# Optimization experiments

Hardware: AMD Instinct MI355X
Metric: run time of the kernel (lower is better)

Reference implementation:

```python
import jax, jax.numpy as jnp
import numpy as np

NF = 64  # n_features
NL = 3   # n_layers


def setup_inputs() -> dict:
    key = jax.random.key(0)
    ks = jax.random.split(key, 16)
    B, G, P = 4, 512, 512
    obs = jax.random.randint(ks[0], (B, G, P), 0, 3).astype(jnp.float32)

    def w(k, shape, fan_in):
        return (jax.random.normal(k, shape, jnp.float32) / np.sqrt(fan_in)).astype(jnp.float32)

    return {
        "obs": obs,
        "W_init_g": w(ks[1], (1, NF), 1),          # node_init_embedding_layer_g Linear(1,64)
        "W_init_p": w(ks[2], (1, NF), 1),
        "W_ee_g": w(ks[3], (1, NF - 1), 1),        # edge_embedding_NN (n_obs_in_p -> 63)
        "W_ef_g": w(ks[4], (NF, NF), NF),          # edge_feature_NN (64 -> 64)
        "W_ee_p": w(ks[5], (1, NF - 1), 1),
        "W_ef_p": w(ks[6], (NF, NF), NF),
        "W_msg_g": w(ks[7], (NL, 2 * NF, NF), 2 * NF),
        "W_upd_g": w(ks[8], (NL, 2 * NF, NF), 2 * NF),
        "W_msg_p": w(ks[9], (NL, 2 * NF, NF), 2 * NF),
        "W_upd_p": w(ks[10], (NL, 2 * NF, NF), 2 * NF),
        "W_pool_g": w(ks[11], (NF, NF), NF),
        "W_pool_p": w(ks[12], (NF, NF), NF),
        "W_ro": w(ks[13], (2 * NF, 1), 2 * NF),    # readout Linear(128,1,bias=True)
        "b_ro": jnp.zeros((1,), jnp.float32),
    }


def _norms(a):
    # torch get_normalisation is under no_grad
    n = jax.lax.stop_gradient(jnp.sum(a != 0, axis=-1, keepdims=True).astype(a.dtype))
    return n, jnp.where(n == 0, 1.0, n)


def _edge_emb(node_feat_opp, adj, norm, nf1, W_ee, W_ef):
    # node_feat_opp: [B,C,1], adj: [B,R,C] -> edge tensor [B,R,C,1]
    mask = (adj != 0).astype(adj.dtype)
    ef = node_feat_opp[:, None, :, :] * mask[..., None]          # [B,R,C,1]
    ee = jax.nn.relu(jnp.einsum('brci,ie->brce', ef, W_ee))      # [B,R,C,63]
    emb = ee.sum(axis=2) / nf1                                   # [B,R,63]
    x = jnp.concatenate([emb, norm / jnp.max(nf1)], axis=-1)     # [B,R,64]
    return jax.nn.relu(x @ W_ef)


def reference(obs, W_init_g, W_init_p, W_ee_g, W_ef_g, W_ee_p, W_ef_p,
              W_msg_g, W_upd_g, W_msg_p, W_upd_p, W_pool_g, W_pool_p, W_ro, b_ro):
    relu = jax.nn.relu
    adj = obs                                  # n_obs_in_g == 1 -> no leading node features
    adjT = jnp.swapaxes(adj, -1, -2)
    B, G, P = adj.shape
    norm_g, nf1_g = _norms(adj)
    norm_p, nf1_p = _norms(adjT)
    nf_g = norm_g / P                          # node_features_g [B,G,1]
    nf_p = norm_p / G                          # node_features_p [B,P,1]
    h_g = relu(nf_g @ W_init_g)                # [B,G,64]
    h_p = relu(nf_p @ W_init_p)                # [B,P,64]
    e_g = _edge_emb(nf_p, adj, norm_g, nf1_g, W_ee_g, W_ef_g)
    e_p = _edge_emb(nf_g, adjT, norm_p, nf1_p, W_ee_p, W_ef_p)
    for i in range(NL):
        agg_g = (adj @ h_p) / nf1_g
        agg_p = (adjT @ h_g) / nf1_p
        m_g = relu(jnp.concatenate([agg_g, e_g], axis=-1) @ W_msg_g[i])
        m_p = relu(jnp.concatenate([agg_p, e_p], axis=-1) @ W_msg_p[i])
        h_g_new = relu(jnp.concatenate([h_g, m_g], axis=-1) @ W_upd_g[i])
        h_p_new = relu(jnp.concatenate([h_p, m_p], axis=-1) @ W_upd_p[i])
        h_g, h_p = h_g_new, h_p_new
    hp_g = (h_g.sum(axis=1) / G) @ W_pool_g    # [B,64]
    hp_p = (h_p.sum(axis=1) / P) @ W_pool_p
    hp = relu(hp_g + hp_p)
    f_pooled = jnp.broadcast_to(hp[:, None, :], h_g.shape)
    feats = relu(jnp.concatenate([f_pooled, h_g], axis=-1))      # [B,G,128]
    out = feats @ W_ro + b_ro                  # [B,G,1]
    return out[..., 0]                         # torch .squeeze() -> [B,G]
```

## Files before the change

### kernel.cpp

```cpp
#include <hip/hip_runtime.h>

#define NF 64

#define OFF_U       8194
#define OFF_NPG     9216
#define OFF_NPP     25600
#define OFF_HA_G    41984
#define OFF_HA_P    173056
#define OFF_HB_G    304128
#define OFF_HB_P    435200
#define OFF_EG      566272
#define OFF_EP      697344
#define OFF_AFRAG   2162688
#define OFF_HFA     3211264
#define OFF_HFB     3735552
#define OFF_WF      4259840
#define OFF_HPART   4358144

typedef __attribute__((ext_vector_type(8))) short bf16x8;
typedef __attribute__((ext_vector_type(4))) float f32x4;

static __device__ __forceinline__ float wave_sum(float v) {
    for (int off = 32; off; off >>= 1) v += __shfl_down(v, off, 64);
    return v;
}
static __device__ __forceinline__ float wave_max(float v) {
    for (int off = 32; off; off >>= 1) v = fmaxf(v, __shfl_down(v, off, 64));
    return v;
}
static __device__ __forceinline__ unsigned short f2bf(float x) {
    unsigned u = __float_as_uint(x);
    return (unsigned short)((u + 0x7FFFu + ((u >> 16) & 1u)) >> 16);
}

__global__ __launch_bounds__(256) void k_prep(const float* __restrict__ obs,
        float* __restrict__ ws,
        const float* __restrict__ Wm_g, const float* __restrict__ Wu_g,
        const float* __restrict__ Wm_p, const float* __restrict__ Wu_p,
        const float* __restrict__ Wee_g, const float* __restrict__ Wef_g,
        const float* __restrict__ Wee_p, const float* __restrict__ Wef_p) {
    __shared__ float tile[64][65];
    __shared__ float cc[4][64];
    int b = blockIdx.y, t = threadIdx.x;
    int tg = blockIdx.x >> 3, tp = blockIdx.x & 7;
    int g0 = tg * 64, p0 = tp * 64;
    int c = t & 63, q = t >> 6;
    const float* src = obs + ((size_t)b * 512 + g0) * 512 + p0;
    float colcnt = 0.f;
#pragma unroll
    for (int i = 0; i < 16; ++i) {
        int r = q + 4 * i;
        float v = src[(size_t)r * 512 + c];
        tile[r][c] = v;
        bool nz = (v != 0.f);
        colcnt += nz ? 1.f : 0.f;
        unsigned long long mask = __ballot(nz);
        if (c == 0)
            ws[OFF_NPG + tp * 2048 + b * 512 + g0 + r] = (float)__popcll(mask);
    }
    cc[q][c] = colcnt;
    __syncthreads();
    if (q == 0)
        ws[OFF_NPP + tg * 2048 + b * 512 + p0 + c] =
            cc[0][c] + cc[1][c] + cc[2][c] + cc[3][c];
    int ri = c & 15, kq = c >> 4;
    unsigned short* afg = (unsigned short*)(ws + OFF_AFRAG);
    unsigned short* afp = afg + 1048576;
    int rt_g = b * 32 + tg * 4 + q;
    int rt_p = b * 32 + tp * 4 + q;
#pragma unroll
    for (int ks2 = 0; ks2 < 2; ++ks2) {
        int ks_g = tp * 2 + ks2;
        int ks_p = tg * 2 + ks2;
        bf16x8 og, op;
#pragma unroll
        for (int i = 0; i < 8; ++i) {
            og[i] = (short)f2bf(tile[q * 16 + ri][ks2 * 32 + kq * 8 + i]);
            op[i] = (short)f2bf(tile[ks2 * 32 + kq * 8 + i][q * 16 + ri]);
        }
        *(bf16x8*)(afg + ((size_t)(rt_g * 16 + ks_g) * 64 + c) * 8) = og;
        *(bf16x8*)(afp + ((size_t)(rt_p * 16 + ks_p) * 64 + c) * 8) = op;
    }
    int lin = b * 64 + blockIdx.x;
    if (lin < 48) {
        int mat = lin >> 2, ks2 = lin & 3;
        int side = mat / 6, m = (mat / 3) & 1, layer = mat % 3;
        const float* W = (side ? (m ? Wu_p : Wm_p) : (m ? Wu_g : Wm_g)) + layer * 8192;
        int ftq = t >> 6, lane = t & 63;
        int f = ftq * 16 + (lane & 15);
        int kbase = ks2 * 32 + ((lane >> 4) & 3) * 8;
        bf16x8 oh, ol;
#pragma unroll
        for (int i = 0; i < 8; ++i) {
            float v = W[(kbase + i) * 64 + f];
            unsigned short hi = f2bf(v);
            oh[i] = (short)hi;
            ol[i] = (short)f2bf(v - __uint_as_float((unsigned)hi << 16));
        }
        unsigned short* WF = (unsigned short*)(ws + OFF_WF);
        *(bf16x8*)(WF + (((size_t)(mat * 2 + 0) * 4 + ks2) * 4 + ftq) * 512 + lane * 8) = oh;
        *(bf16x8*)(WF + (((size_t)(mat * 2 + 1) * 4 + ks2) * 4 + ftq) * 512 + lane * 8) = ol;
    } else if (lin == 48 && t < 128) {
        int side = t >> 6, f = t & 63;
        const float* Wee = side ? Wee_p : Wee_g;
        const float* Wef = side ? Wef_p : Wef_g;
        float u = 0.f;
#pragma unroll
        for (int e = 0; e < 63; ++e) u += fmaxf(Wee[e], 0.f) * Wef[e * 64 + f];
        ws[OFF_U + t] = u;
    }
}

__global__ __launch_bounds__(256) void k_init_l0(float* __restrict__ ws,
        const float* __restrict__ Wi_g, const float* __restrict__ Wi_p,
        const float* __restrict__ Wef_g, const float* __restrict__ Wef_p) {
    __shared__ float normall[2048];
    __shared__ float nopp[512];
    __shared__ float redm[4];
    __shared__ float sred[4][16], wred[4][16];
    __shared__ float s_l[16], w_l[16];
    __shared__ float xe[16][68], xh[16][68], xa[16][68], xm[16][68];
    int bid = blockIdx.x, side = bid >> 7, rt = bid & 127;
    int lr0 = rt * 16, b = rt >> 5;
    int t = threadIdx.x, lane = t & 63, w = t >> 6;
    const float* pown = ws + (side ? OFF_NPP : OFF_NPG);
    const float* popp = ws + (side ? OFF_NPG : OFF_NPP) + b * 512;
#pragma unroll
    for (int i = 0; i < 8; ++i) {
        int r = t + 256 * i;
        float s = 0.f;
#pragma unroll
        for (int j = 0; j < 8; ++j) s += pown[j * 2048 + r];
        normall[r] = s;
    }
#pragma unroll
    for (int i = 0; i < 2; ++i) {
        int r = t + 256 * i;
        float s = 0.f;
#pragma unroll
        for (int j = 0; j < 8; ++j) s += popp[j * 2048 + r];
        nopp[r] = s;
    }
    __syncthreads();
    float m = 0.f;
#pragma unroll
    for (int i = 0; i < 8; ++i) m = fmaxf(m, normall[t + 256 * i]);
    m = wave_max(m);
    if (lane == 0) redm[w] = m;
    const unsigned short* af = (const unsigned short*)(ws + OFF_AFRAG)
                               + (size_t)side * 1048576;
    int kq = lane >> 4;
    float sacc = 0.f, wacc = 0.f;
#pragma unroll
    for (int kk = 0; kk < 4; ++kk) {
        int ks = w * 4 + kk;
        bf16x8 a = *(const bf16x8*)(af + ((size_t)(rt * 16 + ks) * 64 + lane) * 8);
#pragma unroll
        for (int i = 0; i < 8; ++i)
            if (a[i] != 0) {
                float nv = nopp[ks * 32 + kq * 8 + i];
                sacc += nv;
                float av = __uint_as_float((unsigned)(unsigned short)a[i] << 16);
                wacc += av * nv;
            }
    }
    sacc += __shfl_xor(sacc, 16, 64);
    sacc += __shfl_xor(sacc, 32, 64);
    wacc += __shfl_xor(wacc, 16, 64);
    wacc += __shfl_xor(wacc, 32, 64);
    if (lane < 16) { sred[w][lane] = sacc; wred[w][lane] = wacc; }
    __syncthreads();
    float mxs = fmaxf(fmaxf(redm[0], redm[1]), fmaxf(redm[2], redm[3]));
    if (t < 16) {
        s_l[t] = (sred[0][t] + sred[1][t] + sred[2][t] + sred[3][t]) * (1.f / 512.f);
        w_l[t] = (wred[0][t] + wred[1][t] + wred[2][t] + wred[3][t]) * (1.f / 512.f);
    }
    __syncthreads();
    float maxnf = fmaxf(mxs, 1.f);
    const float* Wi_own = side ? Wi_p : Wi_g;
    const float* Wi_opp = side ? Wi_g : Wi_p;
    const float* Wef = side ? Wef_p : Wef_g;
    int ff = lane;
    float Uv = ws[OFF_U + side * 64 + ff];
    float wef63 = Wef[63 * 64 + ff];
    float wiv = Wi_own[ff];
    float wio = fmaxf(Wi_opp[ff], 0.f);
#pragma unroll
    for (int q = 0; q < 4; ++q) {
        int r = w * 4 + q, lr = lr0 + r;
        float norm = normall[lr];
        float nf1 = norm > 0.f ? norm : 1.f;
        float h = fmaxf(norm * (1.f / 512.f) * wiv, 0.f);
        xh[r][ff] = h;
        float A = s_l[r] / nf1;
        float C = norm / maxnf;
        float e = fmaxf(A * Uv + C * wef63, 0.f);
        ws[(side ? OFF_EP : OFF_EG) + (size_t)lr * 64 + ff] = e;
        xe[r][ff] = e;
        xa[r][ff] = w_l[r] * wio / nf1;
    }
    __syncthreads();

    int ft = __builtin_amdgcn_readfirstlane(w);
    const unsigned short* WF = (const unsigned short*)(ws + OFF_WF);
    int mat_msg = (side * 2 + 0) * 3 + 0;
    int mat_upd = (side * 2 + 1) * 3 + 0;
    int ar = lane & 15, koff = ((lane >> 4) & 3) * 8;

    f32x4 mc = {0.f, 0.f, 0.f, 0.f};
#pragma unroll
    for (int ks2 = 0; ks2 < 4; ++ks2) {
        const float* src = (ks2 < 2) ? &xa[ar][ks2 * 32 + koff]
                                     : &xe[ar][(ks2 - 2) * 32 + koff];
        float4 lo4 = *(const float4*)src;
        float4 hi4 = *(const float4*)(src + 4);
        bf16x8 xhf, xlf;
        {
            float xv[8] = {lo4.x, lo4.y, lo4.z, lo4.w, hi4.x, hi4.y, hi4.z, hi4.w};
#pragma unroll
            for (int i = 0; i < 8; ++i) {
                unsigned short hh = f2bf(xv[i]);
                xhf[i] = (short)hh;
                xlf[i] = (short)f2bf(xv[i] - __uint_as_float((unsigned)hh << 16));
            }
        }
        bf16x8 wh = *(const bf16x8*)(WF + (((size_t)(mat_msg * 2 + 0) * 4 + ks2) * 4 + ft) * 512 + lane * 8);
        bf16x8 wl = *(const bf16x8*)(WF + (((size_t)(mat_msg * 2 + 1) * 4 + ks2) * 4 + ft) * 512 + lane * 8);
        mc = __builtin_amdgcn_mfma_f32_16x16x32_bf16(xhf, wh, mc, 0, 0, 0);
        mc = __builtin_amdgcn_mfma_f32_16x16x32_bf16(xlf, wh, mc, 0, 0, 0);
        mc = __builtin_amdgcn_mfma_f32_16x16x32_bf16(xhf, wl, mc, 0, 0, 0);
    }
    {
        int c = lane & 15, rq = (lane >> 4) * 4, f = ft * 16 + c;
#pragma unroll
        for (int j = 0; j < 4; ++j) xm[rq + j][f] = fmaxf(mc[j], 0.f);
    }
    __syncthreads();

    f32x4 uc = {0.f, 0.f, 0.f, 0.f};
#pragma unroll
    for (int ks2 = 0; ks2 < 4; ++ks2) {
        const float* src = (ks2 < 2) ? &xh[ar][ks2 * 32 + koff]
                                     : &xm[ar][(ks2 - 2) * 32 + koff];
        float4 lo4 = *(const float4*)src;
        float4 hi4 = *(const float4*)(src + 4);
        bf16x8 xhf, xlf;
        {
            float xv[8] = {lo4.x, lo4.y, lo4.z, lo4.w, hi4.x, hi4.y, hi4.z, hi4.w};
#pragma unroll
            for (int i = 0; i < 8; ++i) {
                unsigned short hh = f2bf(xv[i]);
                xhf[i] = (short)hh;
                xlf[i] = (short)f2bf(xv[i] - __uint_as_float((unsigned)hh << 16));
            }
        }
        bf16x8 wh = *(const bf16x8*)(WF + (((size_t)(mat_upd * 2 + 0) * 4 + ks2) * 4 + ft) * 512 + lane * 8);
        bf16x8 wl = *(const bf16x8*)(WF + (((size_t)(mat_upd * 2 + 1) * 4 + ks2) * 4 + ft) * 512 + lane * 8);
        uc = __builtin_amdgcn_mfma_f32_16x16x32_bf16(xhf, wh, uc, 0, 0, 0);
        uc = __builtin_amdgcn_mfma_f32_16x16x32_bf16(xlf, wh, uc, 0, 0, 0);
        uc = __builtin_amdgcn_mfma_f32_16x16x32_bf16(xhf, wl, uc, 0, 0, 0);
    }
    {
        int c = lane & 15, rq = (lane >> 4) * 4, f = ft * 16 + c;
        int hout = side ? OFF_HB_P : OFF_HB_G;
        unsigned short hi4[4], lo4b[4];
#pragma unroll
        for (int j = 0; j < 4; ++j) {
            float hv = fmaxf(uc[j], 0.f);
            ws[hout + (size_t)(lr0 + rq + j) * 64 + f] = hv;
            unsigned short hh = f2bf(hv);
            hi4[j] = hh;
            lo4b[j] = f2bf(hv - __uint_as_float((unsigned)hh << 16));
        }
        int k0 = (rt & 31) * 16 + rq;
        int ks_h = k0 >> 5;
        int lane2 = (f & 15) | (((k0 >> 3) & 3) << 4);
        size_t fidx = (((size_t)(b * 4 + ft) * 16 + ks_h) * 64 + lane2) * 8 + (k0 & 7);
        unsigned short* hf = (unsigned short*)(ws + OFF_HFB) + (size_t)side * 2 * 262144;
        uint2 vh, vl;
        vh.x = (unsigned)hi4[0] | ((unsigned)hi4[1] << 16);
        vh.y = (unsigned)hi4[2] | ((unsigned)hi4[3] << 16);
        vl.x = (unsigned)lo4b[0] | ((unsigned)lo4b[1] << 16);
        vl.y = (unsigned)lo4b[2] | ((unsigned)lo4b[3] << 16);
        *(uint2*)(hf + fidx) = vh;
        *(uint2*)(hf + 262144 + fidx) = vl;
    }
}

__global__ __launch_bounds__(256) void k_layer(float* __restrict__ ws, int layer,
        int hin_g, int hin_p, int hout_g, int hout_p, int fin, int fout, int do_pool) {
    __shared__ float xe[16][68], xh[16][68], xa[16][68], xm[16][68];
    __shared__ float nrm16[16];
    __shared__ float psum[4][64];
    int bid = blockIdx.x, side = bid >> 7, rt = bid & 127;
    int lr0 = rt * 16, b = rt >> 5;
    int t = threadIdx.x, lane = t & 63;
    int ft = __builtin_amdgcn_readfirstlane(t >> 6);

    {
        int r = t >> 4, c4 = (t & 15) * 4;
        *(float4*)&xe[r][c4] = *(const float4*)(ws + (side ? OFF_EP : OFF_EG)
                                                + (size_t)(lr0 + r) * 64 + c4);
        *(float4*)&xh[r][c4] = *(const float4*)(ws + (side ? hin_p : hin_g)
                                                + (size_t)(lr0 + r) * 64 + c4);
        if (t < 16) {
            const float* po = ws + (side ? OFF_NPP : OFF_NPG) + lr0 + t;
            float s = 0.f;
#pragma unroll
            for (int j = 0; j < 8; ++j) s += po[j * 2048];
            nrm16[t] = fmaxf(s, 1.f);
        }
    }
    __syncthreads();

    const unsigned short* af = (const unsigned short*)(ws + OFF_AFRAG)
                               + (size_t)side * 1048576;
    const unsigned short* hfh = (const unsigned short*)(ws + fin)
                                + (size_t)(1 - side) * 2 * 262144;
    const unsigned short* hfl = hfh + 262144;
    f32x4 acc = {0.f, 0.f, 0.f, 0.f};
#pragma unroll
    for (int ks = 0; ks < 16; ++ks) {
        bf16x8 a = *(const bf16x8*)(af + ((size_t)(rt * 16 + ks) * 64 + lane) * 8);
        size_t bi = ((((size_t)b * 4 + ft) * 16 + ks) * 64 + lane) * 8;
        bf16x8 bh = *(const bf16x8*)(hfh + bi);
        bf16x8 bl = *(const bf16x8*)(hfl + bi);
        acc = __builtin_amdgcn_mfma_f32_16x16x32_bf16(a, bh, acc, 0, 0, 0);
        acc = __builtin_amdgcn_mfma_f32_16x16x32_bf16(a, bl, acc, 0, 0, 0);
    }
    {
        int c = lane & 15, rq = (lane >> 4) * 4, f = ft * 16 + c;
#pragma unroll
        for (int j = 0; j < 4; ++j)
            xa[rq + j][f] = acc[j] / nrm16[rq + j];
    }
    __syncthreads();

    const unsigned short* WF = (const unsigned short*)(ws + OFF_WF);
    int mat_msg = (side * 2 + 0) * 3 + layer;
    int mat_upd = (side * 2 + 1) * 3 + layer;
    int ar = lane & 15, koff = ((lane >> 4) & 3) * 8;

    f32x4 mc = {0.f, 0.f, 0.f, 0.f};
#pragma unroll
    for (int ks2 = 0; ks2 < 4; ++ks2) {
        const float* src = (ks2 < 2) ? &xa[ar][ks2 * 32 + koff]
                                     : &xe[ar][(ks2 - 2) * 32 + koff];
        float4 lo4 = *(const float4*)src;
        float4 hi4 = *(const float4*)(src + 4);
        bf16x8 xhf, xlf;
        {
            float xv[8] = {lo4.x, lo4.y, lo4.z, lo4.w, hi4.x, hi4.y, hi4.z, hi4.w};
#pragma unroll
            for (int i = 0; i < 8; ++i) {
                unsigned short hh = f2bf(xv[i]);
                xhf[i] = (short)hh;
                xlf[i] = (short)f2bf(xv[i] - __uint_as_float((unsigned)hh << 16));
            }
        }
        bf16x8 wh = *(const bf16x8*)(WF + (((size_t)(mat_msg * 2 + 0) * 4 + ks2) * 4 + ft) * 512 + lane * 8);
        bf16x8 wl = *(const bf16x8*)(WF + (((size_t)(mat_msg * 2 + 1) * 4 + ks2) * 4 + ft) * 512 + lane * 8);
        mc = __builtin_amdgcn_mfma_f32_16x16x32_bf16(xhf, wh, mc, 0, 0, 0);
        mc = __builtin_amdgcn_mfma_f32_16x16x32_bf16(xlf, wh, mc, 0, 0, 0);
        mc = __builtin_amdgcn_mfma_f32_16x16x32_bf16(xhf, wl, mc, 0, 0, 0);
    }
    {
        int c = lane & 15, rq = (lane >> 4) * 4, f = ft * 16 + c;
#pragma unroll
        for (int j = 0; j < 4; ++j) xm[rq + j][f] = fmaxf(mc[j], 0.f);
    }
    __syncthreads();

    f32x4 uc = {0.f, 0.f, 0.f, 0.f};
#pragma unroll
    for (int ks2 = 0; ks2 < 4; ++ks2) {
        const float* src = (ks2 < 2) ? &xh[ar][ks2 * 32 + koff]
                                     : &xm[ar][(ks2 - 2) * 32 + koff];
        float4 lo4 = *(const float4*)src;
        float4 hi4 = *(const float4*)(src + 4);
        bf16x8 xhf, xlf;
        {
            float xv[8] = {lo4.x, lo4.y, lo4.z, lo4.w, hi4.x, hi4.y, hi4.z, hi4.w};
#pragma unroll
            for (int i = 0; i < 8; ++i) {
                unsigned short hh = f2bf(xv[i]);
                xhf[i] = (short)hh;
                xlf[i] = (short)f2bf(xv[i] - __uint_as_float((unsigned)hh << 16));
            }
        }
        bf16x8 wh = *(const bf16x8*)(WF + (((size_t)(mat_upd * 2 + 0) * 4 + ks2) * 4 + ft) * 512 + lane * 8);
        bf16x8 wl = *(const bf16x8*)(WF + (((size_t)(mat_upd * 2 + 1) * 4 + ks2) * 4 + ft) * 512 + lane * 8);
        uc = __builtin_amdgcn_mfma_f32_16x16x32_bf16(xhf, wh, uc, 0, 0, 0);
        uc = __builtin_amdgcn_mfma_f32_16x16x32_bf16(xlf, wh, uc, 0, 0, 0);
        uc = __builtin_amdgcn_mfma_f32_16x16x32_bf16(xhf, wl, uc, 0, 0, 0);
    }
    {
        int c = lane & 15, rq = (lane >> 4) * 4, f = ft * 16 + c;
        int hout = side ? hout_p : hout_g;
        float s4 = 0.f;
        unsigned short hi4[4], lo4[4];
#pragma unroll
        for (int j = 0; j < 4; ++j) {
            float hv = fmaxf(uc[j], 0.f);
            ws[hout + (size_t)(lr0 + rq + j) * 64 + f] = hv;
            unsigned short hh = f2bf(hv);
            hi4[j] = hh;
            lo4[j] = f2bf(hv - __uint_as_float((unsigned)hh << 16));
            s4 += hv;
        }
        int k0 = (rt & 31) * 16 + rq;
        int ks_h = k0 >> 5;
        int lane2 = (f & 15) | (((k0 >> 3) & 3) << 4);
        size_t fidx = (((size_t)(b * 4 + ft) * 16 + ks_h) * 64 + lane2) * 8 + (k0 & 7);
        unsigned short* hf = (unsigned short*)(ws + fout) + (size_t)side * 2 * 262144;
        uint2 vh, vl;
        vh.x = (unsigned)hi4[0] | ((unsigned)hi4[1] << 16);
        vh.y = (unsigned)hi4[2] | ((unsigned)hi4[3] << 16);
        vl.x = (unsigned)lo4[0] | ((unsigned)lo4[1] << 16);
        vl.y = (unsigned)lo4[2] | ((unsigned)lo4[3] << 16);
        *(uint2*)(hf + fidx) = vh;
        *(uint2*)(hf + 262144 + fidx) = vl;
        if (do_pool) {
            psum[lane >> 4][f] = s4;
            __syncthreads();
            if (t < 64)
                ws[OFF_HPART + bid * 64 + t] =
                    psum[0][t] + psum[1][t] + psum[2][t] + psum[3][t];
        }
    }
}

__global__ __launch_bounds__(256) void k_out(const float* __restrict__ Wpg,
                                             const float* __restrict__ Wpp,
                                             const float* __restrict__ Wro,
                                             const float* __restrict__ bro,
                                             const float* __restrict__ ws,
                                             float* __restrict__ out) {
    __shared__ float hp[128];
    __shared__ float c1s;
    int bid = blockIdx.x;
    int row0 = bid * 256, b = row0 >> 9;
    int t = threadIdx.x;
    if (t < 128) {
        int sd = t >> 6, k = t & 63;
        const float* q = ws + OFF_HPART + (size_t)(sd * 128 + b * 32) * 64 + k;
        float s = 0.f;
#pragma unroll
        for (int i = 0; i < 32; ++i) s += q[i * 64];
        hp[t] = s;
    }
    __syncthreads();
    if (t < 64) {
        float vg = 0.f, vp = 0.f;
#pragma unroll 4
        for (int k = 0; k < 64; ++k) {
            vg += (hp[k] * (1.f / 512.f)) * Wpg[k * 64 + t];
            vp += (hp[64 + k] * (1.f / 512.f)) * Wpp[k * 64 + t];
        }
        float hv = fmaxf(vg + vp, 0.f);
        float c = wave_sum(hv * Wro[t]);
        if (t == 0) c1s = c + bro[0];
    }
    __syncthreads();
    int idx = row0 + t;
    const float4* hrow = (const float4*)(ws + OFF_HB_G + (size_t)idx * 64);
    float s = 0.f;
#pragma unroll
    for (int k4 = 0; k4 < 16; ++k4) {
        float4 h4 = hrow[k4];
        s += h4.x * Wro[64 + k4 * 4 + 0];
        s += h4.y * Wro[64 + k4 * 4 + 1];
        s += h4.z * Wro[64 + k4 * 4 + 2];
        s += h4.w * Wro[64 + k4 * 4 + 3];
    }
    out[idx] = c1s + s;
}

extern "C" void kernel_launch(void* const* d_in, const int* in_sizes, int n_in,
                              void* d_out, int out_size, void* d_ws, size_t ws_size,
                              hipStream_t stream) {
    const float* obs   = (const float*)d_in[0];
    const float* Wi_g  = (const float*)d_in[1];
    const float* Wi_p  = (const float*)d_in[2];
    const float* Wee_g = (const float*)d_in[3];
    const float* Wef_g = (const float*)d_in[4];
    const float* Wee_p = (const float*)d_in[5];
    const float* Wef_p = (const float*)d_in[6];
    const float* Wm_g  = (const float*)d_in[7];
    const float* Wu_g  = (const float*)d_in[8];
    const float* Wm_p  = (const float*)d_in[9];
    const float* Wu_p  = (const float*)d_in[10];
    const float* Wpg   = (const float*)d_in[11];
    const float* Wpp   = (const float*)d_in[12];
    const float* Wro   = (const float*)d_in[13];
    const float* bro   = (const float*)d_in[14];
    float* ws  = (float*)d_ws;
    float* out = (float*)d_out;

    k_prep<<<dim3(64, 4), 256, 0, stream>>>(obs, ws, Wm_g, Wu_g, Wm_p, Wu_p,
                                            Wee_g, Wef_g, Wee_p, Wef_p);
    k_init_l0<<<256, 256, 0, stream>>>(ws, Wi_g, Wi_p, Wef_g, Wef_p);

    k_layer<<<256, 256, 0, stream>>>(ws, 1, OFF_HB_G, OFF_HB_P, OFF_HA_G, OFF_HA_P,
                                     OFF_HFB, OFF_HFA, 0);
    k_layer<<<256, 256, 0, stream>>>(ws, 2, OFF_HA_G, OFF_HA_P, OFF_HB_G, OFF_HB_P,
                                     OFF_HFA, OFF_HFB, 1);

    k_out<<<8, 256, 0, stream>>>(Wpg, Wpp, Wro, bro, ws, out);
}
```

Measured before the change: 46.88 us.

## Fuse readout kernel into last layer via last-block atomic counter

Removes the separate k_out launch by computing per-row readout dot products inside the final k_layer and having the last block to finish (detected with an atomic counter and release/acquire fences) do the pooling, the small pooled matvec and the final output write. This saves one kernel launch and the reread of h_g. In exchange, one block serially handles the pooling for all four batches and writes 2048 outputs, which adds a tail. The counter is reset in k_prep.

```diff
diff --git a/kernel.cpp b/kernel.cpp
--- a/kernel.cpp
+++ b/kernel.cpp
@@ -16,6 +16,8 @@
 #define OFF_HFB     3735552
 #define OFF_WF      4259840
 #define OFF_HPART   4358144
+#define OFF_CNT     4374528
+#define OFF_RD      4374592
 
 typedef __attribute__((ext_vector_type(8))) short bf16x8;
 typedef __attribute__((ext_vector_type(4))) float f32x4;
@@ -42,6 +44,7 @@
     __shared__ float tile[64][65];
     __shared__ float cc[4][64];
     int b = blockIdx.y, t = threadIdx.x;
+    if (blockIdx.x == 0 && b == 0 && t == 0) ((int*)(ws + OFF_CNT))[0] = 0;
     int tg = blockIdx.x >> 3, tp = blockIdx.x & 7;
     int g0 = tg * 64, p0 = tp * 64;
     int c = t & 63, q = t >> 6;
@@ -288,10 +291,17 @@
 }
 
 __global__ __launch_bounds__(256) void k_layer(float* __restrict__ ws, int layer,
-        int hin_g, int hin_p, int hout_g, int hout_p, int fin, int fout, int do_pool) {
+        int hin_g, int hin_p, int hout_g, int hout_p, int fin, int fout, int do_pool,
+        const float* __restrict__ Wpg, const float* __restrict__ Wpp,
+        const float* __restrict__ Wro, const float* __restrict__ bro,
+        float* __restrict__ out) {
     __shared__ float xe[16][68], xh[16][68], xa[16][68], xm[16][68];
     __shared__ float nrm16[16];
     __shared__ float psum[4][64];
+    __shared__ float rds[16][64];
+    __shared__ float hp2[128];
+    __shared__ float c1v[4];
+    __shared__ int lastflag;
     int bid = blockIdx.x, side = bid >> 7, rt = bid & 127;
     int lr0 = rt * 16, b = rt >> 5;
     int t = threadIdx.x, lane = t & 63;
@@ -398,10 +408,12 @@
         int c = lane & 15, rq = (lane >> 4) * 4, f = ft * 16 + c;
         int hout = side ? hout_p : hout_g;
         float s4 = 0.f;
+        float hvv[4];
         unsigned short hi4[4], lo4[4];
 #pragma unroll
         for (int j = 0; j < 4; ++j) {
             float hv = fmaxf(uc[j], 0.f);
+            hvv[j] = hv;
             ws[hout + (size_t)(lr0 + rq + j) * 64 + f] = hv;
             unsigned short hh = f2bf(hv);
             hi4[j] = hh;
@@ -420,60 +432,63 @@
         vl.y = (unsigned)lo4[2] | ((unsigned)lo4[3] << 16);
         *(uint2*)(hf + fidx) = vh;
         *(uint2*)(hf + 262144 + fidx) = vl;
+
         if (do_pool) {
+            float wro64 = Wro[64 + f];
             psum[lane >> 4][f] = s4;
+#pragma unroll
+            for (int j = 0; j < 4; ++j) rds[rq + j][f] = hvv[j] * wro64;
             __syncthreads();
             if (t < 64)
                 ws[OFF_HPART + bid * 64 + t] =
                     psum[0][t] + psum[1][t] + psum[2][t] + psum[3][t];
-        }
-    }
-}
-
-__global__ __launch_bounds__(256) void k_out(const float* __restrict__ Wpg,
-                                             const float* __restrict__ Wpp,
-                                             const float* __restrict__ Wro,
-                                             const float* __restrict__ bro,
-                                             const float* __restrict__ ws,
-                                             float* __restrict__ out) {
-    __shared__ float hp[128];
-    __shared__ float c1s;
-    int bid = blockIdx.x;
-    int row0 = bid * 256, b = row0 >> 9;
-    int t = threadIdx.x;
-    if (t < 128) {
-        int sd = t >> 6, k = t & 63;
-        const float* q = ws + OFF_HPART + (size_t)(sd * 128 + b * 32) * 64 + k;
-        float s = 0.f;
-#pragma unroll
-        for (int i = 0; i < 32; ++i) s += q[i * 64];
-        hp[t] = s;
-    }
-    __syncthreads();
-    if (t < 64) {
-        float vg = 0.f, vp = 0.f;
+            if (side == 0 && t < 16) {
+                float s = 0.f;
+#pragma unroll
+                for (int k = 0; k < 64; ++k) s += rds[t][k];
+                ws[OFF_RD + lr0 + t] = s;
+            }
+            __builtin_amdgcn_fence(__ATOMIC_RELEASE, "agent");
+            __syncthreads();
+            if (t == 0) {
+                int old = __hip_atomic_fetch_add((int*)(ws + OFF_CNT), 1,
+                                                 __ATOMIC_ACQ_REL, __HIP_MEMORY_SCOPE_AGENT);
+                lastflag = (old == 255) ? 1 : 0;
+            }
+            __syncthreads();
+            if (lastflag) {
+                __builtin_amdgcn_fence(__ATOMIC_ACQUIRE, "agent");
+                for (int b2 = 0; b2 < 4; ++b2) {
+                    if (t < 128) {
+                        int sd = t >> 6, k = t & 63;
+                        const float* qq = ws + OFF_HPART + (size_t)(sd * 128 + b2 * 32) * 64 + k;
+                        float s = 0.f;
+#pragma unroll
+                        for (int i = 0; i < 32; ++i) s += qq[i * 64];
+                        hp2[t] = s;
+                    }
+                    __syncthreads();
+                    if (t < 64) {
+                        float vg = 0.f, vp = 0.f;
 #pragma unroll 4
-        for (int k = 0; k < 64; ++k) {
-            vg += (hp[k] * (1.f / 512.f)) * Wpg[k * 64 + t];
-            vp += (hp[64 + k] * (1.f / 512.f)) * Wpp[k * 64 + t];
-        }
-        float hv = fmaxf(vg + vp, 0.f);
-        float c = wave_sum(hv * Wro[t]);
-        if (t == 0) c1s = c + bro[0];
-    }
-    __syncthreads();
-    int idx = row0 + t;
-    const float4* hrow = (const float4*)(ws + OFF_HB_G + (size_t)idx * 64);
-    float s = 0.f;
-#pragma unroll
-    for (int k4 = 0; k4 < 16; ++k4) {
-        float4 h4 = hrow[k4];
-        s += h4.x * Wro[64 + k4 * 4 + 0];
-        s += h4.y * Wro[64 + k4 * 4 + 1];
-        s += h4.z * Wro[64 + k4 * 4 + 2];
-        s += h4.w * Wro[64 + k4 * 4 + 3];
-    }
-    out[idx] = c1s + s;
+                        for (int k = 0; k < 64; ++k) {
+                            vg += (hp2[k] * (1.f / 512.f)) * Wpg[k * 64 + t];
+                            vp += (hp2[64 + k] * (1.f / 512.f)) * Wpp[k * 64 + t];
+                        }
+                        float hv2 = fmaxf(vg + vp, 0.f);
+                        float cc2 = wave_sum(hv2 * Wro[t]);
+                        if (t == 0) c1v[b2] = cc2 + bro[0];
+                    }
+                    __syncthreads();
+                }
+#pragma unroll
+                for (int i = 0; i < 8; ++i) {
+                    int idx = t + 256 * i;
+                    out[idx] = c1v[idx >> 9] + ws[OFF_RD + idx];
+                }
+            }
+        }
+    }
 }
 
 extern "C" void kernel_launch(void* const* d_in, const int* in_sizes, int n_in,
@@ -502,9 +517,7 @@
     k_init_l0<<<256, 256, 0, stream>>>(ws, Wi_g, Wi_p, Wef_g, Wef_p);
 
     k_layer<<<256, 256, 0, stream>>>(ws, 1, OFF_HB_G, OFF_HB_P, OFF_HA_G, OFF_HA_P,
-                                     OFF_HFB, OFF_HFA, 0);
+                                     OFF_HFB, OFF_HFA, 0, Wpg, Wpp, Wro, bro, out);
     k_layer<<<256, 256, 0, stream>>>(ws, 2, OFF_HA_G, OFF_HA_P, OFF_HB_G, OFF_HB_P,
-                                     OFF_HFA, OFF_HFB, 1);
-
-    k_out<<<8, 256, 0, stream>>>(Wpg, Wpp, Wro, bro, ws, out);
-}
+                                     OFF_HFA, OFF_HFB, 1, Wpg, Wpp, Wro, bro, out);
+}
```

After: 63.86 us. 1.36x slower.
